# Performance work log

Hardware: AMD Instinct MI355X
Metric: run time of the kernel (lower is better)

The kernel has to match this reference:

```python
import jax, jax.numpy as jnp
import numpy as np

EPS = 1e-5

def conv2d(x, w, b=None, pad=1):
    # x: [B,C,H,W], w: [O,I,kh,kw]
    y = jax.lax.conv_general_dilated(x, w, (1, 1), [(pad, pad), (pad, pad)],
                                     dimension_numbers=('NCHW', 'OIHW', 'NCHW'))
    if b is not None:
        y = y + b[None, :, None, None]
    return y

def bn(x, g, b, m, v):
    # inference-mode batchnorm
    inv = g / jnp.sqrt(v + EPS)
    return x * inv[None, :, None, None] + (b - m * inv)[None, :, None, None]

def coord_conv(x, w, b):
    B, C, H, W = x.shape
    yy = jnp.broadcast_to(jnp.linspace(-1.0, 1.0, H)[:, None], (H, W))
    xx = jnp.broadcast_to(jnp.linspace(-1.0, 1.0, W)[None, :], (H, W))
    coords = jnp.broadcast_to(jnp.stack([xx, yy])[None], (B, 2, H, W)).astype(x.dtype)
    return conv2d(jnp.concatenate([x, coords], axis=1), w, b, pad=1)

def deform_conv(x, offset, w):
    # deformable conv v1, 3x3, pad=1, stride=1, no bias
    B, C, H, W = x.shape
    K = 9
    # offset channels interleaved (y, x) per kernel tap
    off = offset.reshape(B, K, 2, H, W)
    off_y, off_x = off[:, :, 0], off[:, :, 1]          # [B,9,H,W]
    k = jnp.arange(K)
    ko_y = (k // 3 - 1).astype(x.dtype)[None, :, None, None]
    ko_x = (k % 3 - 1).astype(x.dtype)[None, :, None, None]
    base_y = jnp.arange(H, dtype=x.dtype)[None, None, :, None]
    base_x = jnp.arange(W, dtype=x.dtype)[None, None, None, :]
    py = base_y + ko_y + off_y                          # [B,9,H,W]
    px = base_x + ko_x + off_x
    xf = x.reshape(B, C, H * W)
    y0 = jnp.floor(py)
    x0 = jnp.floor(px)
    acc = jnp.zeros((B, C, K, H, W), x.dtype)
    for dy in (0.0, 1.0):
        for dx in (0.0, 1.0):
            yy = y0 + dy
            xx = x0 + dx
            wgt = (1.0 - jnp.abs(py - yy)) * (1.0 - jnp.abs(px - xx))
            valid = (yy >= 0) & (yy < H) & (xx >= 0) & (xx < W)
            wgt = jnp.where(valid, wgt, 0.0)            # zero padding OOB
            yi = jnp.clip(yy, 0, H - 1).astype(jnp.int32)
            xi = jnp.clip(xx, 0, W - 1).astype(jnp.int32)
            idx = (yi * W + xi).reshape(B, K * H * W)
            v = jnp.take_along_axis(xf, idx[:, None, :], axis=2).reshape(B, C, K, H, W)
            acc = acc + v * wgt[:, None]
    wk = w.reshape(w.shape[0], w.shape[1], K)           # [O,I,9]
    return jnp.einsum('bckhw,ock->bohw', acc, wk)

def setup_inputs() -> dict:
    key = jax.random.key(0)
    ks = jax.random.split(key, 16)
    d_model, hd = 256, 64
    B, H, W = 8, 96, 96
    f32 = jnp.float32
    def bn_params(k):
        k1, k2, k3 = jax.random.split(k, 3)
        return (1.0 + 0.1 * jax.random.normal(k1, (hd,), f32),
                0.1 * jax.random.normal(k2, (hd,), f32),
                0.1 * jax.random.normal(k3, (hd,), f32),
                0.5 + jax.random.uniform(jax.random.fold_in(k, 7), (hd,), f32))
    bn1 = bn_params(ks[1]); bn2 = bn_params(ks[2]); bn3 = bn_params(ks[3]); bn4 = bn_params(ks[4])
    inp = {
        'features': jax.random.normal(ks[0], (B, H, W, d_model), f32),
        'coord_w': 0.05 * jax.random.normal(ks[5], (hd, d_model + 2, 3, 3), f32),
        'coord_b': jnp.zeros((hd,), f32),
        'bn1_g': bn1[0], 'bn1_b': bn1[1], 'bn1_m': bn1[2], 'bn1_v': bn1[3],
        'off_w': 0.01 * jax.random.normal(ks[6], (18, hd, 3, 3), f32),
        'off_b': 0.01 * jax.random.normal(ks[7], (18,), f32),
        'dc_w': 0.05 * jax.random.normal(ks[8], (hd, hd, 3, 3), f32),
        'bn2_g': bn2[0], 'bn2_b': bn2[1], 'bn2_m': bn2[2], 'bn2_v': bn2[3],
        'r1_w': 0.05 * jax.random.normal(ks[9], (hd, hd, 3, 3), f32),
        'bn3_g': bn3[0], 'bn3_b': bn3[1], 'bn3_m': bn3[2], 'bn3_v': bn3[3],
        'r2_w': 0.05 * jax.random.normal(ks[10], (hd, hd, 3, 3), f32),
        'bn4_g': bn4[0], 'bn4_b': bn4[1], 'bn4_m': bn4[2], 'bn4_v': bn4[3],
        'out_w': 0.1 * jax.random.normal(ks[11], (1, hd, 1, 1), f32),
        'out_b': jnp.zeros((1,), f32),
    }
    return inp

def reference(features, coord_w, coord_b, bn1_g, bn1_b, bn1_m, bn1_v,
              off_w, off_b, dc_w, bn2_g, bn2_b, bn2_m, bn2_v,
              r1_w, bn3_g, bn3_b, bn3_m, bn3_v,
              r2_w, bn4_g, bn4_b, bn4_m, bn4_v, out_w, out_b):
    x = jnp.transpose(features, (0, 3, 1, 2))           # NHWC -> NCHW
    x = jax.nn.relu(bn(coord_conv(x, coord_w, coord_b), bn1_g, bn1_b, bn1_m, bn1_v))
    offset = conv2d(x, off_w, off_b, pad=1)
    x = deform_conv(x, offset, dc_w)
    x = jax.nn.relu(bn(x, bn2_g, bn2_b, bn2_m, bn2_v))
    x = jax.nn.relu(bn(conv2d(x, r1_w, None, pad=1), bn3_g, bn3_b, bn3_m, bn3_v))
    x = jax.nn.relu(bn(conv2d(x, r2_w, None, pad=1), bn4_g, bn4_b, bn4_m, bn4_v))
    return jax.nn.sigmoid(conv2d(x, out_w, out_b, pad=0))
```

## Files before the change

kernel.cpp:

```cpp
#include <hip/hip_runtime.h>


typedef unsigned short u16;
typedef unsigned int u32;
typedef __attribute__((ext_vector_type(8))) short bf16x8;
typedef __attribute__((ext_vector_type(4))) float f32x4;

#define EPSBN 1e-5f

__device__ __forceinline__ u16 f2bf(float f) {
  u32 u = __builtin_bit_cast(u32, f);
  u32 r = u + 0x7FFFu + ((u >> 16) & 1u);
  return (u16)(r >> 16);
}
__device__ __forceinline__ float lo2f(u32 w) { return __builtin_bit_cast(float, w << 16); }
__device__ __forceinline__ float hi2f(u32 w) { return __builtin_bit_cast(float, w & 0xFFFF0000u); }


#define SEG_X0   4718592
#define SEG_WCF  147456
#define SEG_WOF  18432
#define SEG_W64  36864
#define SEG_CXY  1152
#define SEG_TOT  (SEG_X0 + SEG_WCF + SEG_WOF + 3*SEG_W64 + SEG_CXY)

__global__ __launch_bounds__(256) void prep_kernel(
    const float* __restrict__ features, const float* __restrict__ coord_w,
    const float* __restrict__ off_w, const float* __restrict__ dc_w,
    const float* __restrict__ r1_w, const float* __restrict__ r2_w,
    u16* __restrict__ x0b, u16* __restrict__ wcf, u16* __restrict__ wof,
    u16* __restrict__ wdf, u16* __restrict__ wr1, u16* __restrict__ wr2,
    float* __restrict__ wcx, float* __restrict__ wcy)
{
  for (long long i = (long long)blockIdx.x * 256 + threadIdx.x; i < SEG_TOT;
       i += (long long)gridDim.x * 256) {
    long long d = i;
    if (d < SEG_X0) {
      float4 f = ((const float4*)features)[d];
      ushort4 u;
      u.x = f2bf(f.x); u.y = f2bf(f.y); u.z = f2bf(f.z); u.w = f2bf(f.w);
      ((ushort4*)x0b)[d] = u;
      continue;
    }
    d -= SEG_X0;
    if (d < SEG_WCF) {
      int j = d & 7, lane = (d >> 3) & 63, o = (d >> 9) & 3;
      int ick = (d >> 11) & 7, tap = (int)(d >> 14);
      int ic = ick * 32 + ((lane >> 4) << 3) + j;
      int oc = o * 16 + (lane & 15);
      wcf[d] = f2bf(coord_w[((size_t)oc * 258 + ic) * 9 + tap]);
      continue;
    }
    d -= SEG_WCF;
    if (d < SEG_WOF) {
      int j = d & 7, lane = (d >> 3) & 63, o = (d >> 9) & 1;
      int ick = (d >> 10) & 1, tap = (int)(d >> 11);
      int ic = ick * 32 + ((lane >> 4) << 3) + j;
      int oc = o * 16 + (lane & 15);
      wof[d] = (oc < 18) ? f2bf(off_w[((size_t)oc * 64 + ic) * 9 + tap]) : (u16)0;
      continue;
    }
    d -= SEG_WOF;
    if (d < 3 * SEG_W64) {
      int seg = (int)(d / SEG_W64);
      long long e = d - (long long)seg * SEG_W64;
      int j = e & 7, lane = (e >> 3) & 63, o = (e >> 9) & 3;
      int ick = (e >> 11) & 1, tap = (int)(e >> 12);
      int ic = ick * 32 + ((lane >> 4) << 3) + j;
      int oc = o * 16 + (lane & 15);
      const float* src = (seg == 0) ? dc_w : (seg == 1) ? r1_w : r2_w;
      u16* dst = (seg == 0) ? wdf : (seg == 1) ? wr1 : wr2;
      dst[e] = f2bf(src[((size_t)oc * 64 + ic) * 9 + tap]);
      continue;
    }
    d -= 3 * SEG_W64;
    if (d < 576) {
      int tap = (int)(d >> 6), oc = (int)(d & 63);
      wcx[d] = coord_w[((size_t)oc * 258 + 256) * 9 + tap];
    } else {
      long long e = d - 576;
      int tap = (int)(e >> 6), oc = (int)(e & 63);
      wcy[e] = coord_w[((size_t)oc * 258 + 257) * 9 + tap];
    }
  }
}

__global__ __launch_bounds__(256, 4) void coord_conv_kernel(
    const u16* __restrict__ x0b, const u16* __restrict__ wcf,
    const float* __restrict__ wcx, const float* __restrict__ wcy,
    const float* __restrict__ cb,
    const float* __restrict__ g, const float* __restrict__ bb,
    const float* __restrict__ m, const float* __restrict__ v,
    u16* __restrict__ x1b)
{
  __shared__ __align__(16) u16 tile[6 * 18 * 72];
  const int t = threadIdx.x;
  const int wv = t >> 6, lane = t & 63;
  const int col = lane & 15, quad = lane >> 4;
  const int o0 = (wv & 1) * 2, m0 = (wv >> 1) * 2;
  const int x0 = blockIdx.x * 16, y0 = blockIdx.y * 4, b = blockIdx.z;

  const f32x4 zf = {0.f, 0.f, 0.f, 0.f};
  f32x4 acc[2][2] = {{zf, zf}, {zf, zf}};

  for (int icc = 0; icc < 4; ++icc) {
    __syncthreads();
    for (int i = t; i < 864; i += 256) {
      const int px = i >> 3, part = i & 7;
      const int ly = px / 18, lx = px - ly * 18;
      const int gy = y0 + ly - 1, gx = x0 + lx - 1;
      uint4 val = {0u, 0u, 0u, 0u};
      if ((unsigned)gy < 96u && (unsigned)gx < 96u)
        val = *(const uint4*)(x0b + (((size_t)((b * 96 + gy) * 96 + gx)) << 8)
                              + icc * 64 + part * 8);
      *(uint4*)(tile + (ly * 18 + lx) * 72 + part * 8) = val;
    }
    __syncthreads();
    #pragma unroll
    for (int tap = 0; tap < 9; ++tap) {
      const int dy = tap / 3, dx = tap - dy * 3;
      #pragma unroll
      for (int half = 0; half < 2; ++half) {
        const int ick = icc * 2 + half;
        bf16x8 bfr[2], afr[2];
        #pragma unroll
        for (int ot = 0; ot < 2; ++ot)
          bfr[ot] = *(const bf16x8*)(wcf +
              ((size_t)((tap * 8 + ick) * 4 + o0 + ot)) * 512 + lane * 8);
        #pragma unroll
        for (int mt = 0; mt < 2; ++mt)
          afr[mt] = *(const bf16x8*)(tile +
              ((m0 + mt + dy) * 18 + col + dx) * 72 + half * 32 + quad * 8);
        #pragma unroll
        for (int mt = 0; mt < 2; ++mt)
          #pragma unroll
          for (int ot = 0; ot < 2; ++ot)
            acc[mt][ot] = __builtin_amdgcn_mfma_f32_16x16x32_bf16(
                afr[mt], bfr[ot], acc[mt][ot], 0, 0, 0);
      }
    }
  }

  #pragma unroll
  for (int ot = 0; ot < 2; ++ot) {
    const int oc = (o0 + ot) * 16 + col;
    const float inv = g[oc] * rsqrtf(v[oc] + EPSBN);
    const float sh = bb[oc] - m[oc] * inv + cb[oc] * inv;
    #pragma unroll
    for (int mt = 0; mt < 2; ++mt) {
      const int y = y0 + m0 + mt;
      #pragma unroll
      for (int r = 0; r < 4; ++r) {
        const int x = x0 + quad * 4 + r;
        float val = acc[mt][ot][r];
        #pragma unroll
        for (int tap = 0; tap < 9; ++tap) {
          const int sy = y + tap / 3 - 1, sx = x + tap % 3 - 1;
          if ((unsigned)sy < 96u && (unsigned)sx < 96u)
            val += wcx[tap * 64 + oc] * (-1.f + (2.f / 95.f) * (float)sx)
                 + wcy[tap * 64 + oc] * (-1.f + (2.f / 95.f) * (float)sy);
        }
        val = fmaxf(fmaf(val, inv, sh), 0.f);
        x1b[((size_t)((b * 96 + y) * 96 + x)) * 64 + oc] = f2bf(val);
      }
    }
  }
}

template<int NOCT, int EPI>
__global__ __launch_bounds__(256, 4) void conv64_kernel(
    const u16* __restrict__ xin, const u16* __restrict__ wf,
    const float* __restrict__ bias,
    const float* __restrict__ g, const float* __restrict__ bb,
    const float* __restrict__ m, const float* __restrict__ v,
    const float* __restrict__ ow, const float* __restrict__ ob,
    void* __restrict__ outp)
{
  __shared__ __align__(16) u16 tile[6 * 18 * 72];
  __shared__ float red[64];
  const int t = threadIdx.x;
  const int wv = t >> 6, lane = t & 63;
  const int col = lane & 15, quad = lane >> 4;
  constexpr int OW = (NOCT == 4) ? 2 : 1;
  const int o0 = (NOCT == 4) ? (wv & 1) * 2 : (wv & 1);
  const int m0 = (wv >> 1) * 2;
  const int x0 = blockIdx.x * 16, y0 = blockIdx.y * 4, b = blockIdx.z;

  if constexpr (EPI == 2) { if (t < 64) red[t] = 0.f; }

  for (int i = t; i < 864; i += 256) {
    const int px = i >> 3, part = i & 7;
    const int ly = px / 18, lx = px - ly * 18;
    const int gy = y0 + ly - 1, gx = x0 + lx - 1;
    uint4 val = {0u, 0u, 0u, 0u};
    if ((unsigned)gy < 96u && (unsigned)gx < 96u)
      val = *(const uint4*)(xin + (((size_t)((b * 96 + gy) * 96 + gx)) << 6)
                            + part * 8);
    *(uint4*)(tile + (ly * 18 + lx) * 72 + part * 8) = val;
  }
  __syncthreads();

  const f32x4 zf = {0.f, 0.f, 0.f, 0.f};
  f32x4 acc[2][OW];
  #pragma unroll
  for (int a = 0; a < 2; ++a)
    #pragma unroll
    for (int o = 0; o < OW; ++o) acc[a][o] = zf;

  #pragma unroll
  for (int tap = 0; tap < 9; ++tap) {
    const int dy = tap / 3, dx = tap - dy * 3;
    #pragma unroll
    for (int half = 0; half < 2; ++half) {
      bf16x8 bfr[OW], afr[2];
      #pragma unroll
      for (int ot = 0; ot < OW; ++ot)
        bfr[ot] = *(const bf16x8*)(wf +
            ((size_t)((tap * 2 + half) * NOCT + o0 + ot)) * 512 + lane * 8);
      #pragma unroll
      for (int mt = 0; mt < 2; ++mt)
        afr[mt] = *(const bf16x8*)(tile +
            ((m0 + mt + dy) * 18 + col + dx) * 72 + half * 32 + quad * 8);
      #pragma unroll
      for (int mt = 0; mt < 2; ++mt)
        #pragma unroll
        for (int ot = 0; ot < OW; ++ot)
          acc[mt][ot] = __builtin_amdgcn_mfma_f32_16x16x32_bf16(
              afr[mt], bfr[ot], acc[mt][ot], 0, 0, 0);
    }
  }

  if constexpr (EPI == 0) {
    u16* xo = (u16*)outp;
    #pragma unroll
    for (int ot = 0; ot < OW; ++ot) {
      const int oc = (o0 + ot) * 16 + col;
      const float inv = g[oc] * rsqrtf(v[oc] + EPSBN);
      const float sh = bb[oc] - m[oc] * inv;
      #pragma unroll
      for (int mt = 0; mt < 2; ++mt) {
        const int y = y0 + m0 + mt;
        #pragma unroll
        for (int r = 0; r < 4; ++r) {
          const int x = x0 + quad * 4 + r;
          const float val = fmaxf(fmaf(acc[mt][ot][r], inv, sh), 0.f);
          xo[((size_t)((b * 96 + y) * 96 + x)) * 64 + oc] = f2bf(val);
        }
      }
    }
  } else if constexpr (EPI == 1) {
    float* fo = (float*)outp;
    const int oc = o0 * 16 + col;
    if (oc < 18) {
      const float bs = bias[oc];
      #pragma unroll
      for (int mt = 0; mt < 2; ++mt) {
        const int y = y0 + m0 + mt;
        #pragma unroll
        for (int r = 0; r < 4; ++r) {
          const int x = x0 + quad * 4 + r;
          fo[((size_t)((b * 96 + y) * 96 + x)) * 18 + oc] = acc[mt][0][r] + bs;
        }
      }
    }
  } else {
    float pr[2][4];
    #pragma unroll
    for (int mt = 0; mt < 2; ++mt)
      #pragma unroll
      for (int r = 0; r < 4; ++r) pr[mt][r] = 0.f;
    #pragma unroll
    for (int ot = 0; ot < OW; ++ot) {
      const int oc = (o0 + ot) * 16 + col;
      const float inv = g[oc] * rsqrtf(v[oc] + EPSBN);
      const float sh = bb[oc] - m[oc] * inv;
      const float wo = ow[oc];
      #pragma unroll
      for (int mt = 0; mt < 2; ++mt)
        #pragma unroll
        for (int r = 0; r < 4; ++r) {
          const float val = fmaxf(fmaf(acc[mt][ot][r], inv, sh), 0.f);
          pr[mt][r] = fmaf(val, wo, pr[mt][r]);
        }
    }
    #pragma unroll
    for (int mask = 1; mask <= 8; mask <<= 1)
      #pragma unroll
      for (int mt = 0; mt < 2; ++mt)
        #pragma unroll
        for (int r = 0; r < 4; ++r)
          pr[mt][r] += __shfl_xor(pr[mt][r], mask);
    if (col == 0) {
      #pragma unroll
      for (int mt = 0; mt < 2; ++mt)
        #pragma unroll
        for (int r = 0; r < 4; ++r)
          atomicAdd(&red[(m0 + mt) * 16 + quad * 4 + r], pr[mt][r]);
    }
    __syncthreads();
    if (t < 64) {
      float* fo = (float*)outp;
      const int y = y0 + (t >> 4), x = x0 + (t & 15);
      const float val = red[t] + ob[0];
      fo[(size_t)(b * 96 + y) * 96 + x] = 1.f / (1.f + expf(-val));
    }
  }
}

__global__ __launch_bounds__(256, 4) void deform_kernel(
    const u16* __restrict__ x1b, const float* __restrict__ off,
    const u16* __restrict__ wdf,
    const float* __restrict__ g, const float* __restrict__ bb,
    const float* __restrict__ m, const float* __restrict__ v,
    u16* __restrict__ x2b)
{
  __shared__ __align__(16) u16 s[64 * 72];
  __shared__ float offs[64 * 18];
  const int t = threadIdx.x;
  const int wv = t >> 6, lane = t & 63;
  const int col = lane & 15, quad = lane >> 4;
  const int o0 = (wv & 1) * 2, m0 = (wv >> 1) * 2;
  const int x0 = blockIdx.x * 16, y0 = blockIdx.y * 4, b = blockIdx.z;

  for (int i = t; i < 64 * 18; i += 256) {
    const int p = i / 18, c = i - p * 18;
    const int gy = y0 + (p >> 4), gx = x0 + (p & 15);
    offs[i] = off[((size_t)((b * 96 + gy) * 96 + gx)) * 18 + c];
  }

  const int sp_px = t >> 2, sp_part = t & 3;
  const int sh_y = y0 + (sp_px >> 4), sh_x = x0 + (sp_px & 15);

  const f32x4 zf = {0.f, 0.f, 0.f, 0.f};
  f32x4 acc[2][2] = {{zf, zf}, {zf, zf}};

  for (int k = 0; k < 9; ++k) {
    __syncthreads();
    {
      const float oy = offs[sp_px * 18 + 2 * k];
      const float ox = offs[sp_px * 18 + 2 * k + 1];
      const float py = (float)(sh_y + k / 3 - 1) + oy;
      const float px = (float)(sh_x + k % 3 - 1) + ox;
      const float yf = floorf(py), xf = floorf(px);
      const float fy = py - yf, fx = px - xf;
      const int yi = (int)yf, xi = (int)xf;
      float val[16];
      #pragma unroll
      for (int j = 0; j < 16; ++j) val[j] = 0.f;
      #pragma unroll
      for (int c4 = 0; c4 < 4; ++c4) {
        const int cy = yi + (c4 >> 1), cx = xi + (c4 & 1);
        if ((unsigned)cy < 96u && (unsigned)cx < 96u) {
          const float wy = (c4 & 2) ? fy : 1.f - fy;
          const float wx = (c4 & 1) ? fx : 1.f - fx;
          const float wgt = wy * wx;
          const u16* spn = x1b + ((size_t)((b * 96 + cy) * 96 + cx)) * 64
                           + sp_part * 16;
          const uint4 ua = *(const uint4*)spn;
          const uint4 ub = *(const uint4*)(spn + 8);
          const u32 uu[8] = {ua.x, ua.y, ua.z, ua.w, ub.x, ub.y, ub.z, ub.w};
          #pragma unroll
          for (int u = 0; u < 8; ++u) {
            val[2 * u]     = fmaf(wgt, lo2f(uu[u]), val[2 * u]);
            val[2 * u + 1] = fmaf(wgt, hi2f(uu[u]), val[2 * u + 1]);
          }
        }
      }
      u32 pk[8];
      #pragma unroll
      for (int u = 0; u < 8; ++u)
        pk[u] = (u32)f2bf(val[2 * u]) | ((u32)f2bf(val[2 * u + 1]) << 16);
      uint4 w0 = {pk[0], pk[1], pk[2], pk[3]};
      uint4 w1 = {pk[4], pk[5], pk[6], pk[7]};
      *(uint4*)(s + sp_px * 72 + sp_part * 16) = w0;
      *(uint4*)(s + sp_px * 72 + sp_part * 16 + 8) = w1;
    }
    __syncthreads();
    #pragma unroll
    for (int half = 0; half < 2; ++half) {
      bf16x8 bfr[2], afr[2];
      #pragma unroll
      for (int ot = 0; ot < 2; ++ot)
        bfr[ot] = *(const bf16x8*)(wdf +
            ((size_t)((k * 2 + half) * 4 + o0 + ot)) * 512 + lane * 8);
      #pragma unroll
      for (int mt = 0; mt < 2; ++mt)
        afr[mt] = *(const bf16x8*)(s + ((m0 + mt) * 16 + col) * 72
                                   + half * 32 + quad * 8);
      #pragma unroll
      for (int mt = 0; mt < 2; ++mt)
        #pragma unroll
        for (int ot = 0; ot < 2; ++ot)
          acc[mt][ot] = __builtin_amdgcn_mfma_f32_16x16x32_bf16(
              afr[mt], bfr[ot], acc[mt][ot], 0, 0, 0);
    }
  }

  #pragma unroll
  for (int ot = 0; ot < 2; ++ot) {
    const int oc = (o0 + ot) * 16 + col;
    const float inv = g[oc] * rsqrtf(v[oc] + EPSBN);
    const float sh = bb[oc] - m[oc] * inv;
    #pragma unroll
    for (int mt = 0; mt < 2; ++mt) {
      const int y = y0 + m0 + mt;
      #pragma unroll
      for (int r = 0; r < 4; ++r) {
        const int x = x0 + quad * 4 + r;
        const float val = fmaxf(fmaf(acc[mt][ot][r], inv, sh), 0.f);
        x2b[((size_t)((b * 96 + y) * 96 + x)) * 64 + oc] = f2bf(val);
      }
    }
  }
}

extern "C" void kernel_launch(void* const* d_in, const int* in_sizes, int n_in,
                              void* d_out, int out_size, void* d_ws,
                              size_t ws_size, hipStream_t stream)
{
  (void)in_sizes; (void)n_in; (void)out_size; (void)ws_size;
  const float* features = (const float*)d_in[0];
  const float* coord_w  = (const float*)d_in[1];
  const float* coord_b  = (const float*)d_in[2];
  const float* bn1g = (const float*)d_in[3];
  const float* bn1b = (const float*)d_in[4];
  const float* bn1m = (const float*)d_in[5];
  const float* bn1v = (const float*)d_in[6];
  const float* off_w = (const float*)d_in[7];
  const float* off_b = (const float*)d_in[8];
  const float* dc_w  = (const float*)d_in[9];
  const float* bn2g = (const float*)d_in[10];
  const float* bn2b = (const float*)d_in[11];
  const float* bn2m = (const float*)d_in[12];
  const float* bn2v = (const float*)d_in[13];
  const float* r1_w = (const float*)d_in[14];
  const float* bn3g = (const float*)d_in[15];
  const float* bn3b = (const float*)d_in[16];
  const float* bn3m = (const float*)d_in[17];
  const float* bn3v = (const float*)d_in[18];
  const float* r2_w = (const float*)d_in[19];
  const float* bn4g = (const float*)d_in[20];
  const float* bn4b = (const float*)d_in[21];
  const float* bn4m = (const float*)d_in[22];
  const float* bn4v = (const float*)d_in[23];
  const float* out_w = (const float*)d_in[24];
  const float* out_b = (const float*)d_in[25];

  char* W = (char*)d_ws;
  u16*   x0b  = (u16*)W;
  float* offb = (float*)W;
  u16*   x3b  = (u16*)(W + 8388608);
  u16*   x1b  = (u16*)(W + 37748736);
  u16*   x2b  = (u16*)(W + 47185920);
  u16*   wcf  = (u16*)(W + 56623104);
  u16*   wof  = wcf + SEG_WCF;
  u16*   wdf  = wof + SEG_WOF;
  u16*   wr1  = wdf + SEG_W64;
  u16*   wr2  = wr1 + SEG_W64;
  float* wcx  = (float*)(W + 56623104 +
                         2 * (SEG_WCF + SEG_WOF + 3 * SEG_W64));
  float* wcy  = wcx + 576;

  prep_kernel<<<2048, 256, 0, stream>>>(features, coord_w, off_w, dc_w, r1_w,
                                        r2_w, x0b, wcf, wof, wdf, wr1, wr2,
                                        wcx, wcy);

  dim3 grid(6, 24, 8);
  coord_conv_kernel<<<grid, 256, 0, stream>>>(
      x0b, wcf, wcx, wcy, coord_b, bn1g, bn1b, bn1m, bn1v, x1b);
  conv64_kernel<2, 1><<<grid, 256, 0, stream>>>(
      x1b, wof, off_b, nullptr, nullptr, nullptr, nullptr, nullptr, nullptr,
      (void*)offb);
  deform_kernel<<<grid, 256, 0, stream>>>(
      x1b, offb, wdf, bn2g, bn2b, bn2m, bn2v, x2b);
  conv64_kernel<4, 0><<<grid, 256, 0, stream>>>(
      x2b, wr1, nullptr, bn3g, bn3b, bn3m, bn3v, nullptr, nullptr, (void*)x3b);
  conv64_kernel<4, 2><<<grid, 256, 0, stream>>>(
      x3b, wr2, nullptr, bn4g, bn4b, bn4m, bn4v, out_w, out_b, d_out);
}
```

Before: 280.7 us.

## Switch convolutions to 32x32x16 MFMA, fuse feature bf16 cast, fold coords into MFMA

All conv and deform kernels move from 16x16x32 to 32x32x16 bf16 MFMA tiles, with each wave covering a 32-pixel row and larger spatial tiles per block. The separate fp32-to-bf16 pass over the input features is removed: the coord conv reads fp32 features and converts while filling shared memory. The scalar per-pixel coordinate-channel loop is replaced by an extra MFMA pass over a zero-padded 2-channel coordinate tile. Weight repacking matches the new fragment layouts. This cuts memory traffic and epilogue ALU work, but halves the block count, which may reduce occupancy and load balance.

```diff
diff --git a/kernel.cpp b/kernel.cpp
--- a/kernel.cpp
+++ b/kernel.cpp
@@ -3,8 +3,8 @@
 
 typedef unsigned short u16;
 typedef unsigned int u32;
-typedef __attribute__((ext_vector_type(8))) short bf16x8;
-typedef __attribute__((ext_vector_type(4))) float f32x4;
+typedef __attribute__((ext_vector_type(8)))  short bf16x8;
+typedef __attribute__((ext_vector_type(16))) float f32x16;
 
 #define EPSBN 1e-5f
 
@@ -13,161 +13,161 @@
   u32 r = u + 0x7FFFu + ((u >> 16) & 1u);
   return (u16)(r >> 16);
 }
+__device__ __forceinline__ u32 pk2(float a, float b) {
+  return (u32)f2bf(a) | ((u32)f2bf(b) << 16);
+}
 __device__ __forceinline__ float lo2f(u32 w) { return __builtin_bit_cast(float, w << 16); }
 __device__ __forceinline__ float hi2f(u32 w) { return __builtin_bit_cast(float, w & 0xFFFF0000u); }
 
-
-#define SEG_X0   4718592
-#define SEG_WCF  147456
-#define SEG_WOF  18432
-#define SEG_W64  36864
-#define SEG_CXY  1152
-#define SEG_TOT  (SEG_X0 + SEG_WCF + SEG_WOF + 3*SEG_W64 + SEG_CXY)
+#define N_WCF 147456
+#define N_WCC 9216
+#define N_WOF 18432
+#define N_W64 36864
+#define N_ALLW (N_WCF + N_WCC + N_WOF + 3*N_W64)
 
 __global__ __launch_bounds__(256) void prep_kernel(
-    const float* __restrict__ features, const float* __restrict__ coord_w,
-    const float* __restrict__ off_w, const float* __restrict__ dc_w,
-    const float* __restrict__ r1_w, const float* __restrict__ r2_w,
-    u16* __restrict__ x0b, u16* __restrict__ wcf, u16* __restrict__ wof,
-    u16* __restrict__ wdf, u16* __restrict__ wr1, u16* __restrict__ wr2,
-    float* __restrict__ wcx, float* __restrict__ wcy)
+    const float* __restrict__ coord_w, const float* __restrict__ off_w,
+    const float* __restrict__ dc_w, const float* __restrict__ r1_w,
+    const float* __restrict__ r2_w,
+    u16* __restrict__ wcf, u16* __restrict__ wcc, u16* __restrict__ wof,
+    u16* __restrict__ wdf, u16* __restrict__ wr1, u16* __restrict__ wr2)
 {
-  for (long long i = (long long)blockIdx.x * 256 + threadIdx.x; i < SEG_TOT;
-       i += (long long)gridDim.x * 256) {
-    long long d = i;
-    if (d < SEG_X0) {
-      float4 f = ((const float4*)features)[d];
-      ushort4 u;
-      u.x = f2bf(f.x); u.y = f2bf(f.y); u.z = f2bf(f.z); u.w = f2bf(f.w);
-      ((ushort4*)x0b)[d] = u;
-      continue;
-    }
-    d -= SEG_X0;
-    if (d < SEG_WCF) {
-      int j = d & 7, lane = (d >> 3) & 63, o = (d >> 9) & 3;
-      int ick = (d >> 11) & 7, tap = (int)(d >> 14);
-      int ic = ick * 32 + ((lane >> 4) << 3) + j;
-      int oc = o * 16 + (lane & 15);
-      wcf[d] = f2bf(coord_w[((size_t)oc * 258 + ic) * 9 + tap]);
-      continue;
-    }
-    d -= SEG_WCF;
-    if (d < SEG_WOF) {
-      int j = d & 7, lane = (d >> 3) & 63, o = (d >> 9) & 1;
-      int ick = (d >> 10) & 1, tap = (int)(d >> 11);
-      int ic = ick * 32 + ((lane >> 4) << 3) + j;
-      int oc = o * 16 + (lane & 15);
-      wof[d] = (oc < 18) ? f2bf(off_w[((size_t)oc * 64 + ic) * 9 + tap]) : (u16)0;
-      continue;
-    }
-    d -= SEG_WOF;
-    if (d < 3 * SEG_W64) {
-      int seg = (int)(d / SEG_W64);
-      long long e = d - (long long)seg * SEG_W64;
-      int j = e & 7, lane = (e >> 3) & 63, o = (e >> 9) & 3;
-      int ick = (e >> 11) & 1, tap = (int)(e >> 12);
-      int ic = ick * 32 + ((lane >> 4) << 3) + j;
-      int oc = o * 16 + (lane & 15);
-      const float* src = (seg == 0) ? dc_w : (seg == 1) ? r1_w : r2_w;
-      u16* dst = (seg == 0) ? wdf : (seg == 1) ? wr1 : wr2;
-      dst[e] = f2bf(src[((size_t)oc * 64 + ic) * 9 + tap]);
-      continue;
-    }
-    d -= 3 * SEG_W64;
-    if (d < 576) {
-      int tap = (int)(d >> 6), oc = (int)(d & 63);
-      wcx[d] = coord_w[((size_t)oc * 258 + 256) * 9 + tap];
-    } else {
-      long long e = d - 576;
-      int tap = (int)(e >> 6), oc = (int)(e & 63);
-      wcy[e] = coord_w[((size_t)oc * 258 + 257) * 9 + tap];
-    }
-  }
+  int i = blockIdx.x * 256 + threadIdx.x;
+  if (i >= N_ALLW) return;
+  int d = i;
+  if (d < N_WCF) {
+    int j = d & 7, lane = (d >> 3) & 63, frag = d >> 9;
+    int nt = frag & 1, h = (frag >> 1) & 3, tap = (frag >> 3) % 9, cc = (frag >> 3) / 9;
+    int ic = cc * 64 + h * 16 + ((lane >> 5) << 3) + j;
+    int oc = nt * 32 + (lane & 31);
+    wcf[d] = f2bf(coord_w[((size_t)oc * 258 + ic) * 9 + tap]);
+    return;
+  }
+  d -= N_WCF;
+  if (d < N_WCC) {
+    int j = d & 7, lane = (d >> 3) & 63, frag = d >> 9;
+    int nt = frag & 1, tap = frag >> 1;
+    int ic = 256 + ((lane >> 5) << 3) + j;
+    int oc = nt * 32 + (lane & 31);
+    wcc[d] = (ic < 258) ? f2bf(coord_w[((size_t)oc * 258 + ic) * 9 + tap]) : (u16)0;
+    return;
+  }
+  d -= N_WCC;
+  if (d < N_WOF) {
+    int j = d & 7, lane = (d >> 3) & 63, frag = d >> 9;
+    int h = frag & 3, tap = frag >> 2;
+    int ic = h * 16 + ((lane >> 5) << 3) + j;
+    int oc = lane & 31;
+    wof[d] = (oc < 18) ? f2bf(off_w[((size_t)oc * 64 + ic) * 9 + tap]) : (u16)0;
+    return;
+  }
+  d -= N_WOF;
+  int seg = d / N_W64;
+  int e = d - seg * N_W64;
+  int j = e & 7, lane = (e >> 3) & 63, frag = e >> 9;
+  int nt = frag & 1, h = (frag >> 1) & 3, tap = frag >> 3;
+  int ic = h * 16 + ((lane >> 5) << 3) + j;
+  int oc = nt * 32 + (lane & 31);
+  const float* src = (seg == 0) ? dc_w : (seg == 1) ? r1_w : r2_w;
+  u16* dst = (seg == 0) ? wdf : (seg == 1) ? wr1 : wr2;
+  dst[e] = f2bf(src[((size_t)oc * 64 + ic) * 9 + tap]);
 }
 
 __global__ __launch_bounds__(256, 4) void coord_conv_kernel(
-    const u16* __restrict__ x0b, const u16* __restrict__ wcf,
-    const float* __restrict__ wcx, const float* __restrict__ wcy,
-    const float* __restrict__ cb,
+    const float* __restrict__ feat, const u16* __restrict__ wcf,
+    const u16* __restrict__ wcc, const float* __restrict__ cb,
     const float* __restrict__ g, const float* __restrict__ bb,
     const float* __restrict__ m, const float* __restrict__ v,
     u16* __restrict__ x1b)
 {
-  __shared__ __align__(16) u16 tile[6 * 18 * 72];
+  __shared__ __align__(16) u16 tile[6 * 34 * 72];
   const int t = threadIdx.x;
   const int wv = t >> 6, lane = t & 63;
-  const int col = lane & 15, quad = lane >> 4;
-  const int o0 = (wv & 1) * 2, m0 = (wv >> 1) * 2;
-  const int x0 = blockIdx.x * 16, y0 = blockIdx.y * 4, b = blockIdx.z;
-
-  const f32x4 zf = {0.f, 0.f, 0.f, 0.f};
-  f32x4 acc[2][2] = {{zf, zf}, {zf, zf}};
-
-  for (int icc = 0; icc < 4; ++icc) {
+  const int l31 = lane & 31, l5 = lane >> 5;
+  const int x0 = blockIdx.x * 32, y0 = blockIdx.y * 4, b = blockIdx.z;
+
+  f32x16 acc[2] = {};
+
+  for (int cc = 0; cc < 4; ++cc) {
     __syncthreads();
-    for (int i = t; i < 864; i += 256) {
-      const int px = i >> 3, part = i & 7;
-      const int ly = px / 18, lx = px - ly * 18;
+    for (int i = t; i < 1632; i += 256) {
+      const int px = i >> 3, gg = i & 7;
+      const int ly = px / 34, lx = px - ly * 34;
       const int gy = y0 + ly - 1, gx = x0 + lx - 1;
-      uint4 val = {0u, 0u, 0u, 0u};
-      if ((unsigned)gy < 96u && (unsigned)gx < 96u)
-        val = *(const uint4*)(x0b + (((size_t)((b * 96 + gy) * 96 + gx)) << 8)
-                              + icc * 64 + part * 8);
-      *(uint4*)(tile + (ly * 18 + lx) * 72 + part * 8) = val;
+      uint4 o = {0u, 0u, 0u, 0u};
+      if ((unsigned)gy < 96u && (unsigned)gx < 96u) {
+        const float* p = feat + ((size_t)((b * 96 + gy) * 96 + gx)) * 256
+                         + cc * 64 + gg * 8;
+        const float4 f0 = *(const float4*)p;
+        const float4 f1 = *(const float4*)(p + 4);
+        o.x = pk2(f0.x, f0.y); o.y = pk2(f0.z, f0.w);
+        o.z = pk2(f1.x, f1.y); o.w = pk2(f1.z, f1.w);
+      }
+      *(uint4*)(tile + (ly * 34 + lx) * 72 + gg * 8) = o;
     }
     __syncthreads();
     #pragma unroll
     for (int tap = 0; tap < 9; ++tap) {
       const int dy = tap / 3, dx = tap - dy * 3;
       #pragma unroll
-      for (int half = 0; half < 2; ++half) {
-        const int ick = icc * 2 + half;
-        bf16x8 bfr[2], afr[2];
+      for (int h = 0; h < 4; ++h) {
+        const bf16x8 afr = *(const bf16x8*)(tile +
+            ((wv + dy) * 34 + l31 + dx) * 72 + h * 16 + l5 * 8);
         #pragma unroll
-        for (int ot = 0; ot < 2; ++ot)
-          bfr[ot] = *(const bf16x8*)(wcf +
-              ((size_t)((tap * 8 + ick) * 4 + o0 + ot)) * 512 + lane * 8);
-        #pragma unroll
-        for (int mt = 0; mt < 2; ++mt)
-          afr[mt] = *(const bf16x8*)(tile +
-              ((m0 + mt + dy) * 18 + col + dx) * 72 + half * 32 + quad * 8);
-        #pragma unroll
-        for (int mt = 0; mt < 2; ++mt)
-          #pragma unroll
-          for (int ot = 0; ot < 2; ++ot)
-            acc[mt][ot] = __builtin_amdgcn_mfma_f32_16x16x32_bf16(
-                afr[mt], bfr[ot], acc[mt][ot], 0, 0, 0);
-      }
-    }
-  }
-
+        for (int nt = 0; nt < 2; ++nt) {
+          const bf16x8 bfr = *(const bf16x8*)(wcf +
+              ((size_t)((((cc * 9 + tap) * 4 + h) * 2) + nt)) * 512 + lane * 8);
+          acc[nt] = __builtin_amdgcn_mfma_f32_32x32x16_bf16(afr, bfr, acc[nt],
+                                                            0, 0, 0);
+        }
+      }
+    }
+  }
+
+  __syncthreads();
+  for (int i = t; i < 408; i += 256) {
+    const int px = i >> 1, gg = i & 1;
+    const int ly = px / 34, lx = px - ly * 34;
+    const int gy = y0 + ly - 1, gx = x0 + lx - 1;
+    uint4 o = {0u, 0u, 0u, 0u};
+    if (gg == 0 && (unsigned)gy < 96u && (unsigned)gx < 96u) {
+      const float xx = -1.f + (2.f / 95.f) * (float)gx;
+      const float yy = -1.f + (2.f / 95.f) * (float)gy;
+      o.x = pk2(xx, yy);
+    }
+    *(uint4*)(tile + (ly * 34 + lx) * 72 + gg * 8) = o;
+  }
+  __syncthreads();
   #pragma unroll
-  for (int ot = 0; ot < 2; ++ot) {
-    const int oc = (o0 + ot) * 16 + col;
+  for (int tap = 0; tap < 9; ++tap) {
+    const int dy = tap / 3, dx = tap - dy * 3;
+    const bf16x8 afr = *(const bf16x8*)(tile +
+        ((wv + dy) * 34 + l31 + dx) * 72 + l5 * 8);
+    #pragma unroll
+    for (int nt = 0; nt < 2; ++nt) {
+      const bf16x8 bfr = *(const bf16x8*)(wcc +
+          ((size_t)(tap * 2 + nt)) * 512 + lane * 8);
+      acc[nt] = __builtin_amdgcn_mfma_f32_32x32x16_bf16(afr, bfr, acc[nt],
+                                                        0, 0, 0);
+    }
+  }
+
+  const int y = y0 + wv;
+  #pragma unroll
+  for (int nt = 0; nt < 2; ++nt) {
+    const int oc = nt * 32 + l31;
     const float inv = g[oc] * rsqrtf(v[oc] + EPSBN);
     const float sh = bb[oc] - m[oc] * inv + cb[oc] * inv;
     #pragma unroll
-    for (int mt = 0; mt < 2; ++mt) {
-      const int y = y0 + m0 + mt;
-      #pragma unroll
-      for (int r = 0; r < 4; ++r) {
-        const int x = x0 + quad * 4 + r;
-        float val = acc[mt][ot][r];
-        #pragma unroll
-        for (int tap = 0; tap < 9; ++tap) {
-          const int sy = y + tap / 3 - 1, sx = x + tap % 3 - 1;
-          if ((unsigned)sy < 96u && (unsigned)sx < 96u)
-            val += wcx[tap * 64 + oc] * (-1.f + (2.f / 95.f) * (float)sx)
-                 + wcy[tap * 64 + oc] * (-1.f + (2.f / 95.f) * (float)sy);
-        }
-        val = fmaxf(fmaf(val, inv, sh), 0.f);
-        x1b[((size_t)((b * 96 + y) * 96 + x)) * 64 + oc] = f2bf(val);
-      }
-    }
-  }
-}
-
-template<int NOCT, int EPI>
+    for (int r = 0; r < 16; ++r) {
+      const int xr = (r & 3) + 8 * (r >> 2) + 4 * l5;
+      const float val = fmaxf(fmaf(acc[nt][r], inv, sh), 0.f);
+      x1b[((size_t)((b * 96 + y) * 96 + x0 + xr)) * 64 + oc] = f2bf(val);
+    }
+  }
+}
+
+template<int NN, int EPI>
 __global__ __launch_bounds__(256, 4) void conv64_kernel(
     const u16* __restrict__ xin, const u16* __restrict__ wf,
     const float* __restrict__ bias,
@@ -176,133 +176,103 @@
     const float* __restrict__ ow, const float* __restrict__ ob,
     void* __restrict__ outp)
 {
-  __shared__ __align__(16) u16 tile[6 * 18 * 72];
-  __shared__ float red[64];
+  __shared__ __align__(16) u16 tile[6 * 34 * 72];
+  __shared__ float red[128];
   const int t = threadIdx.x;
   const int wv = t >> 6, lane = t & 63;
-  const int col = lane & 15, quad = lane >> 4;
-  constexpr int OW = (NOCT == 4) ? 2 : 1;
-  const int o0 = (NOCT == 4) ? (wv & 1) * 2 : (wv & 1);
-  const int m0 = (wv >> 1) * 2;
-  const int x0 = blockIdx.x * 16, y0 = blockIdx.y * 4, b = blockIdx.z;
-
-  if constexpr (EPI == 2) { if (t < 64) red[t] = 0.f; }
-
-  for (int i = t; i < 864; i += 256) {
-    const int px = i >> 3, part = i & 7;
-    const int ly = px / 18, lx = px - ly * 18;
+  const int l31 = lane & 31, l5 = lane >> 5;
+  const int x0 = blockIdx.x * 32, y0 = blockIdx.y * 4, b = blockIdx.z;
+
+  for (int i = t; i < 1632; i += 256) {
+    const int px = i >> 3, gg = i & 7;
+    const int ly = px / 34, lx = px - ly * 34;
     const int gy = y0 + ly - 1, gx = x0 + lx - 1;
-    uint4 val = {0u, 0u, 0u, 0u};
+    uint4 o = {0u, 0u, 0u, 0u};
     if ((unsigned)gy < 96u && (unsigned)gx < 96u)
-      val = *(const uint4*)(xin + (((size_t)((b * 96 + gy) * 96 + gx)) << 6)
-                            + part * 8);
-    *(uint4*)(tile + (ly * 18 + lx) * 72 + part * 8) = val;
+      o = *(const uint4*)(xin + (((size_t)((b * 96 + gy) * 96 + gx)) << 6)
+                          + gg * 8);
+    *(uint4*)(tile + (ly * 34 + lx) * 72 + gg * 8) = o;
   }
   __syncthreads();
 
-  const f32x4 zf = {0.f, 0.f, 0.f, 0.f};
-  f32x4 acc[2][OW];
-  #pragma unroll
-  for (int a = 0; a < 2; ++a)
-    #pragma unroll
-    for (int o = 0; o < OW; ++o) acc[a][o] = zf;
-
+  f32x16 acc[NN] = {};
   #pragma unroll
   for (int tap = 0; tap < 9; ++tap) {
     const int dy = tap / 3, dx = tap - dy * 3;
     #pragma unroll
-    for (int half = 0; half < 2; ++half) {
-      bf16x8 bfr[OW], afr[2];
-      #pragma unroll
-      for (int ot = 0; ot < OW; ++ot)
-        bfr[ot] = *(const bf16x8*)(wf +
-            ((size_t)((tap * 2 + half) * NOCT + o0 + ot)) * 512 + lane * 8);
-      #pragma unroll
-      for (int mt = 0; mt < 2; ++mt)
-        afr[mt] = *(const bf16x8*)(tile +
-            ((m0 + mt + dy) * 18 + col + dx) * 72 + half * 32 + quad * 8);
-      #pragma unroll
-      for (int mt = 0; mt < 2; ++mt)
-        #pragma unroll
-        for (int ot = 0; ot < OW; ++ot)
-          acc[mt][ot] = __builtin_amdgcn_mfma_f32_16x16x32_bf16(
-              afr[mt], bfr[ot], acc[mt][ot], 0, 0, 0);
-    }
-  }
-
+    for (int h = 0; h < 4; ++h) {
+      const bf16x8 afr = *(const bf16x8*)(tile +
+          ((wv + dy) * 34 + l31 + dx) * 72 + h * 16 + l5 * 8);
+      #pragma unroll
+      for (int nt = 0; nt < NN; ++nt) {
+        const bf16x8 bfr = *(const bf16x8*)(wf +
+            ((size_t)((tap * 4 + h) * NN + nt)) * 512 + lane * 8);
+        acc[nt] = __builtin_amdgcn_mfma_f32_32x32x16_bf16(afr, bfr, acc[nt],
+                                                          0, 0, 0);
+      }
+    }
+  }
+
+  const int y = y0 + wv;
   if constexpr (EPI == 0) {
     u16* xo = (u16*)outp;
     #pragma unroll
-    for (int ot = 0; ot < OW; ++ot) {
-      const int oc = (o0 + ot) * 16 + col;
+    for (int nt = 0; nt < NN; ++nt) {
+      const int oc = nt * 32 + l31;
       const float inv = g[oc] * rsqrtf(v[oc] + EPSBN);
       const float sh = bb[oc] - m[oc] * inv;
       #pragma unroll
-      for (int mt = 0; mt < 2; ++mt) {
-        const int y = y0 + m0 + mt;
-        #pragma unroll
-        for (int r = 0; r < 4; ++r) {
-          const int x = x0 + quad * 4 + r;
-          const float val = fmaxf(fmaf(acc[mt][ot][r], inv, sh), 0.f);
-          xo[((size_t)((b * 96 + y) * 96 + x)) * 64 + oc] = f2bf(val);
-        }
+      for (int r = 0; r < 16; ++r) {
+        const int xr = (r & 3) + 8 * (r >> 2) + 4 * l5;
+        const float val = fmaxf(fmaf(acc[nt][r], inv, sh), 0.f);
+        xo[((size_t)((b * 96 + y) * 96 + x0 + xr)) * 64 + oc] = f2bf(val);
       }
     }
   } else if constexpr (EPI == 1) {
     float* fo = (float*)outp;
-    const int oc = o0 * 16 + col;
+    const int oc = l31;
     if (oc < 18) {
       const float bs = bias[oc];
       #pragma unroll
-      for (int mt = 0; mt < 2; ++mt) {
-        const int y = y0 + m0 + mt;
-        #pragma unroll
-        for (int r = 0; r < 4; ++r) {
-          const int x = x0 + quad * 4 + r;
-          fo[((size_t)((b * 96 + y) * 96 + x)) * 18 + oc] = acc[mt][0][r] + bs;
-        }
+      for (int r = 0; r < 16; ++r) {
+        const int xr = (r & 3) + 8 * (r >> 2) + 4 * l5;
+        fo[((size_t)((b * 96 + y) * 96 + x0 + xr)) * 18 + oc] = acc[0][r] + bs;
       }
     }
   } else {
-    float pr[2][4];
-    #pragma unroll
-    for (int mt = 0; mt < 2; ++mt)
-      #pragma unroll
-      for (int r = 0; r < 4; ++r) pr[mt][r] = 0.f;
-    #pragma unroll
-    for (int ot = 0; ot < OW; ++ot) {
-      const int oc = (o0 + ot) * 16 + col;
+    float pr[16];
+    #pragma unroll
+    for (int r = 0; r < 16; ++r) pr[r] = 0.f;
+    #pragma unroll
+    for (int nt = 0; nt < NN; ++nt) {
+      const int oc = nt * 32 + l31;
       const float inv = g[oc] * rsqrtf(v[oc] + EPSBN);
       const float sh = bb[oc] - m[oc] * inv;
       const float wo = ow[oc];
       #pragma unroll
-      for (int mt = 0; mt < 2; ++mt)
-        #pragma unroll
-        for (int r = 0; r < 4; ++r) {
-          const float val = fmaxf(fmaf(acc[mt][ot][r], inv, sh), 0.f);
-          pr[mt][r] = fmaf(val, wo, pr[mt][r]);
-        }
-    }
-    #pragma unroll
-    for (int mask = 1; mask <= 8; mask <<= 1)
-      #pragma unroll
-      for (int mt = 0; mt < 2; ++mt)
-        #pragma unroll
-        for (int r = 0; r < 4; ++r)
-          pr[mt][r] += __shfl_xor(pr[mt][r], mask);
-    if (col == 0) {
-      #pragma unroll
-      for (int mt = 0; mt < 2; ++mt)
-        #pragma unroll
-        for (int r = 0; r < 4; ++r)
-          atomicAdd(&red[(m0 + mt) * 16 + quad * 4 + r], pr[mt][r]);
+      for (int r = 0; r < 16; ++r) {
+        const float val = fmaxf(fmaf(acc[nt][r], inv, sh), 0.f);
+        pr[r] = fmaf(val, wo, pr[r]);
+      }
+    }
+    #pragma unroll
+    for (int mask = 1; mask <= 16; mask <<= 1)
+      #pragma unroll
+      for (int r = 0; r < 16; ++r)
+        pr[r] += __shfl_xor(pr[r], mask);
+    if (l31 == 0) {
+      #pragma unroll
+      for (int r = 0; r < 16; ++r) {
+        const int xr = (r & 3) + 8 * (r >> 2) + 4 * l5;
+        red[wv * 32 + xr] = pr[r];
+      }
     }
     __syncthreads();
-    if (t < 64) {
+    if (t < 128) {
       float* fo = (float*)outp;
-      const int y = y0 + (t >> 4), x = x0 + (t & 15);
+      const int yy = y0 + (t >> 5), xx = x0 + (t & 31);
       const float val = red[t] + ob[0];
-      fo[(size_t)(b * 96 + y) * 96 + x] = 1.f / (1.f + expf(-val));
+      fo[(size_t)(b * 96 + yy) * 96 + xx] = 1.f / (1.f + expf(-val));
     }
   }
 }
@@ -314,33 +284,32 @@
     const float* __restrict__ m, const float* __restrict__ v,
     u16* __restrict__ x2b)
 {
-  __shared__ __align__(16) u16 s[64 * 72];
-  __shared__ float offs[64 * 18];
+  __shared__ __align__(16) u16 s[128 * 72];
+  __shared__ float offs[128 * 18];
   const int t = threadIdx.x;
   const int wv = t >> 6, lane = t & 63;
-  const int col = lane & 15, quad = lane >> 4;
-  const int o0 = (wv & 1) * 2, m0 = (wv >> 1) * 2;
-  const int x0 = blockIdx.x * 16, y0 = blockIdx.y * 4, b = blockIdx.z;
-
-  for (int i = t; i < 64 * 18; i += 256) {
+  const int l31 = lane & 31, l5 = lane >> 5;
+  const int x0 = blockIdx.x * 16, y0 = blockIdx.y * 8, b = blockIdx.z;
+
+  for (int i = t; i < 2304; i += 256) {
     const int p = i / 18, c = i - p * 18;
     const int gy = y0 + (p >> 4), gx = x0 + (p & 15);
     offs[i] = off[((size_t)((b * 96 + gy) * 96 + gx)) * 18 + c];
   }
 
-  const int sp_px = t >> 2, sp_part = t & 3;
-  const int sh_y = y0 + (sp_px >> 4), sh_x = x0 + (sp_px & 15);
-
-  const f32x4 zf = {0.f, 0.f, 0.f, 0.f};
-  f32x4 acc[2][2] = {{zf, zf}, {zf, zf}};
+  f32x16 acc[2] = {};
 
   for (int k = 0; k < 9; ++k) {
     __syncthreads();
-    {
-      const float oy = offs[sp_px * 18 + 2 * k];
-      const float ox = offs[sp_px * 18 + 2 * k + 1];
-      const float py = (float)(sh_y + k / 3 - 1) + oy;
-      const float px = (float)(sh_x + k % 3 - 1) + ox;
+    #pragma unroll
+    for (int rr = 0; rr < 2; ++rr) {
+      const int role = t + rr * 256;
+      const int sp = role >> 2, part = role & 3;
+      const int sy = y0 + (sp >> 4), sx = x0 + (sp & 15);
+      const float oy = offs[sp * 18 + 2 * k];
+      const float ox = offs[sp * 18 + 2 * k + 1];
+      const float py = (float)(sy + k / 3 - 1) + oy;
+      const float px = (float)(sx + k % 3 - 1) + ox;
       const float yf = floorf(py), xf = floorf(px);
       const float fy = py - yf, fx = px - xf;
       const int yi = (int)yf, xi = (int)xf;
@@ -348,16 +317,16 @@
       #pragma unroll
       for (int j = 0; j < 16; ++j) val[j] = 0.f;
       #pragma unroll
-      for (int c4 = 0; c4 < 4; ++c4) {
-        const int cy = yi + (c4 >> 1), cx = xi + (c4 & 1);
+      for (int cor = 0; cor < 4; ++cor) {
+        const int cy = yi + (cor >> 1), cx = xi + (cor & 1);
         if ((unsigned)cy < 96u && (unsigned)cx < 96u) {
-          const float wy = (c4 & 2) ? fy : 1.f - fy;
-          const float wx = (c4 & 1) ? fx : 1.f - fx;
+          const float wy = (cor & 2) ? fy : 1.f - fy;
+          const float wx = (cor & 1) ? fx : 1.f - fx;
           const float wgt = wy * wx;
-          const u16* spn = x1b + ((size_t)((b * 96 + cy) * 96 + cx)) * 64
-                           + sp_part * 16;
-          const uint4 ua = *(const uint4*)spn;
-          const uint4 ub = *(const uint4*)(spn + 8);
+          const u16* sp2 = x1b + ((size_t)((b * 96 + cy) * 96 + cx)) * 64
+                           + part * 16;
+          const uint4 ua = *(const uint4*)sp2;
+          const uint4 ub = *(const uint4*)(sp2 + 8);
           const u32 uu[8] = {ua.x, ua.y, ua.z, ua.w, ub.x, ub.y, ub.z, ub.w};
           #pragma unroll
           for (int u = 0; u < 8; ++u) {
@@ -368,48 +337,38 @@
       }
       u32 pk[8];
       #pragma unroll
-      for (int u = 0; u < 8; ++u)
-        pk[u] = (u32)f2bf(val[2 * u]) | ((u32)f2bf(val[2 * u + 1]) << 16);
+      for (int u = 0; u < 8; ++u) pk[u] = pk2(val[2 * u], val[2 * u + 1]);
       uint4 w0 = {pk[0], pk[1], pk[2], pk[3]};
       uint4 w1 = {pk[4], pk[5], pk[6], pk[7]};
-      *(uint4*)(s + sp_px * 72 + sp_part * 16) = w0;
-      *(uint4*)(s + sp_px * 72 + sp_part * 16 + 8) = w1;
+      *(uint4*)(s + sp * 72 + part * 16) = w0;
+      *(uint4*)(s + sp * 72 + part * 16 + 8) = w1;
     }
     __syncthreads();
     #pragma unroll
-    for (int half = 0; half < 2; ++half) {
-      bf16x8 bfr[2], afr[2];
-      #pragma unroll
-      for (int ot = 0; ot < 2; ++ot)
-        bfr[ot] = *(const bf16x8*)(wdf +
-            ((size_t)((k * 2 + half) * 4 + o0 + ot)) * 512 + lane * 8);
-      #pragma unroll
-      for (int mt = 0; mt < 2; ++mt)
-        afr[mt] = *(const bf16x8*)(s + ((m0 + mt) * 16 + col) * 72
-                                   + half * 32 + quad * 8);
-      #pragma unroll
-      for (int mt = 0; mt < 2; ++mt)
-        #pragma unroll
-        for (int ot = 0; ot < 2; ++ot)
-          acc[mt][ot] = __builtin_amdgcn_mfma_f32_16x16x32_bf16(
-              afr[mt], bfr[ot], acc[mt][ot], 0, 0, 0);
+    for (int h = 0; h < 4; ++h) {
+      const bf16x8 afr = *(const bf16x8*)(s + (wv * 32 + l31) * 72
+                                          + h * 16 + l5 * 8);
+      #pragma unroll
+      for (int nt = 0; nt < 2; ++nt) {
+        const bf16x8 bfr = *(const bf16x8*)(wdf +
+            ((size_t)((k * 4 + h) * 2 + nt)) * 512 + lane * 8);
+        acc[nt] = __builtin_amdgcn_mfma_f32_32x32x16_bf16(afr, bfr, acc[nt],
+                                                          0, 0, 0);
+      }
     }
   }
 
   #pragma unroll
-  for (int ot = 0; ot < 2; ++ot) {
-    const int oc = (o0 + ot) * 16 + col;
+  for (int nt = 0; nt < 2; ++nt) {
+    const int oc = nt * 32 + l31;
     const float inv = g[oc] * rsqrtf(v[oc] + EPSBN);
     const float sh = bb[oc] - m[oc] * inv;
     #pragma unroll
-    for (int mt = 0; mt < 2; ++mt) {
-      const int y = y0 + m0 + mt;
-      #pragma unroll
-      for (int r = 0; r < 4; ++r) {
-        const int x = x0 + quad * 4 + r;
-        const float val = fmaxf(fmaf(acc[mt][ot][r], inv, sh), 0.f);
-        x2b[((size_t)((b * 96 + y) * 96 + x)) * 64 + oc] = f2bf(val);
-      }
+    for (int r = 0; r < 16; ++r) {
+      const int pxi = wv * 32 + (r & 3) + 8 * (r >> 2) + 4 * l5;
+      const int y = y0 + (pxi >> 4), x = x0 + (pxi & 15);
+      const float val = fmaxf(fmaf(acc[nt][r], inv, sh), 0.f);
+      x2b[((size_t)((b * 96 + y) * 96 + x)) * 64 + oc] = f2bf(val);
     }
   }
 }
@@ -447,34 +406,32 @@
   const float* out_b = (const float*)d_in[25];
 
   char* W = (char*)d_ws;
-  u16*   x0b  = (u16*)W;
   float* offb = (float*)W;
-  u16*   x3b  = (u16*)(W + 8388608);
-  u16*   x1b  = (u16*)(W + 37748736);
-  u16*   x2b  = (u16*)(W + 47185920);
-  u16*   wcf  = (u16*)(W + 56623104);
-  u16*   wof  = wcf + SEG_WCF;
-  u16*   wdf  = wof + SEG_WOF;
-  u16*   wr1  = wdf + SEG_W64;
-  u16*   wr2  = wr1 + SEG_W64;
-  float* wcx  = (float*)(W + 56623104 +
-                         2 * (SEG_WCF + SEG_WOF + 3 * SEG_W64));
-  float* wcy  = wcx + 576;
-
-  prep_kernel<<<2048, 256, 0, stream>>>(features, coord_w, off_w, dc_w, r1_w,
-                                        r2_w, x0b, wcf, wof, wdf, wr1, wr2,
-                                        wcx, wcy);
-
-  dim3 grid(6, 24, 8);
+  u16*   x1b  = (u16*)(W + 5308416);
+  u16*   x2b  = (u16*)(W + 14745600);
+  u16*   x3b  = (u16*)(W + 24182784);
+  u16*   wcf  = (u16*)(W + 33619968);
+  u16*   wcc  = wcf + N_WCF;
+  u16*   wof  = wcc + N_WCC;
+  u16*   wdf  = wof + N_WOF;
+  u16*   wr1  = wdf + N_W64;
+  u16*   wr2  = wr1 + N_W64;
+
+  prep_kernel<<<(N_ALLW + 255) / 256, 256, 0, stream>>>(
+      coord_w, off_w, dc_w, r1_w, r2_w, wcf, wcc, wof, wdf, wr1, wr2);
+
+  dim3 grid(3, 24, 8);
+  dim3 gridD(6, 12, 8);
+
   coord_conv_kernel<<<grid, 256, 0, stream>>>(
-      x0b, wcf, wcx, wcy, coord_b, bn1g, bn1b, bn1m, bn1v, x1b);
-  conv64_kernel<2, 1><<<grid, 256, 0, stream>>>(
+      features, wcf, wcc, coord_b, bn1g, bn1b, bn1m, bn1v, x1b);
+  conv64_kernel<1, 1><<<grid, 256, 0, stream>>>(
       x1b, wof, off_b, nullptr, nullptr, nullptr, nullptr, nullptr, nullptr,
       (void*)offb);
-  deform_kernel<<<grid, 256, 0, stream>>>(
+  deform_kernel<<<gridD, 256, 0, stream>>>(
       x1b, offb, wdf, bn2g, bn2b, bn2m, bn2v, x2b);
-  conv64_kernel<4, 0><<<grid, 256, 0, stream>>>(
+  conv64_kernel<2, 0><<<grid, 256, 0, stream>>>(
       x2b, wr1, nullptr, bn3g, bn3b, bn3m, bn3v, nullptr, nullptr, (void*)x3b);
-  conv64_kernel<4, 2><<<grid, 256, 0, stream>>>(
+  conv64_kernel<2, 2><<<grid, 256, 0, stream>>>(
       x3b, wr2, nullptr, bn4g, bn4b, bn4m, bn4v, out_w, out_b, d_out);
 }
```

After: 270.8 us. 3.5% less time.
